# Performance work log

Measured on AMD Instinct MI355X. Metric: run time of the kernel, lower is better.

The kernel has to match this reference:

```python
import jax, jax.numpy as jnp
import numpy as np

N = 50000      # nodes (particles)
E = 1600000    # edges
G = 2000       # graphs (jets)
NEG_SLOPE = 0.2

def setup_inputs() -> dict:
    key = jax.random.key(0)
    ks = jax.random.split(key, 18)
    p = lambda k, s: (jax.random.normal(k, s, jnp.float32) * 0.1)
    return {
        'x': jax.random.normal(ks[0], (N, 3), jnp.float32),
        'edge_index': jax.random.randint(ks[1], (2, E), 0, N, dtype=jnp.int64),
        'batch': jnp.sort(jax.random.randint(ks[2], (N,), 0, G, dtype=jnp.int64)),
        'W1': p(ks[3], (3, 128)),  'a1s': p(ks[4], (4, 32)),  'a1d': p(ks[5], (4, 32)),  'b1': p(ks[6], (128,)),
        'W2': p(ks[7], (128, 128)),'a2s': p(ks[8], (4, 32)),  'a2d': p(ks[9], (4, 32)),  'b2': p(ks[10], (128,)),
        'W3': p(ks[11], (128, 32)),'a3s': p(ks[12], (1, 32)), 'a3d': p(ks[13], (1, 32)), 'b3': p(ks[14], (32,)),
        'Wh': p(ks[15], (32, 2)),  'bh': p(ks[16], (2,)),
    }

def gat_conv(x, src, dst, W, a_src, a_dst, b, concat):
    """PyG GATConv (eval mode): gather-score-softmax-scatter over edges (src->dst)."""
    n = x.shape[0]
    H, C = a_src.shape
    h = (x @ W).reshape(n, H, C)                         # [N,H,C]
    es = jnp.sum(h * a_src, axis=-1)                     # [N,H] source scores
    ed = jnp.sum(h * a_dst, axis=-1)                     # [N,H] dest scores
    e = jax.nn.leaky_relu(es[src] + ed[dst], NEG_SLOPE)  # [E,H]
    # neighbor-wise (per destination node) stable softmax
    m = jax.ops.segment_max(e, dst, num_segments=n)      # [N,H]
    m = jax.lax.stop_gradient(jnp.where(jnp.isfinite(m), m, 0.0))
    w = jnp.exp(e - m[dst])
    z = jax.ops.segment_sum(w, dst, num_segments=n)      # [N,H]
    alpha = w / (z[dst] + 1e-16)                         # [E,H]
    out = jax.ops.segment_sum(h[src] * alpha[:, :, None], dst, num_segments=n)  # [N,H,C]
    out = out.reshape(n, H * C) if concat else out.mean(axis=1)
    return out + b

def reference(x, edge_index, batch, W1, a1s, a1d, b1, W2, a2s, a2d, b2,
              W3, a3s, a3d, b3, Wh, bh):
    n = x.shape[0]
    loops = jnp.arange(n, dtype=edge_index.dtype)        # add_self_loops=True
    src = jnp.concatenate([edge_index[0], loops])
    dst = jnp.concatenate([edge_index[1], loops])
    h = jax.nn.elu(gat_conv(x, src, dst, W1, a1s, a1d, b1, True))
    h = jax.nn.elu(gat_conv(h, src, dst, W2, a2s, a2d, b2, True))
    h = jax.nn.elu(gat_conv(h, src, dst, W3, a3s, a3d, b3, False))
    cnt = jax.ops.segment_sum(jnp.ones((n,), h.dtype), batch, num_segments=G)
    pooled = jax.ops.segment_sum(h, batch, num_segments=G) / jnp.maximum(cnt, 1.0)[:, None]
    return pooled @ Wh + bh                              # [G, n_classes]
```

## Files before the change

kernel.cpp:

```cpp
#include <hip/hip_runtime.h>

#define CAP 80
#define NXCD 8
#define SUBW 128
#define NSUBR 49
#define SQC 96
#define QCAPB 512
#define CHUNK 2048

typedef int vint4 __attribute__((ext_vector_type(4)));
__device__ __forceinline__ vint4 ntload_i4(const int* p){ return __builtin_nontemporal_load((const vint4*)p); }

__device__ __forceinline__ float lrelu02(float x){ return x > 0.f ? x : 0.2f*x; }
__device__ __forceinline__ float eluf(float x){ return x > 0.f ? x : (__expf(x)-1.f); }
__device__ __forceinline__ unsigned short f2bf(float x){
  unsigned u = __float_as_uint(x);
  u += 0x7fffu + ((u >> 16) & 1u);
  return (unsigned short)(u >> 16);
}
__device__ __forceinline__ float bf2f(unsigned short b){
  return __uint_as_float(((unsigned)b) << 16);
}

__global__ void radix_proj1_kernel(const int* __restrict__ src, const int* __restrict__ dst,
                                   int E, int n, int nrb, int RW, int qcap,
                                   int* __restrict__ gcur, int2* __restrict__ qbuf,
                                   const float* __restrict__ x, const float* __restrict__ W,
                                   const float* __restrict__ as_, const float* __restrict__ ad_,
                                   unsigned short* __restrict__ hout, float* __restrict__ es,
                                   float* __restrict__ ed){
  if ((int)blockIdx.x < nrb){
    __shared__ int2 q[NXCD][QCAPB];
    __shared__ int qc[NXCD];
    __shared__ int qbase[NXCD];
    int t = threadIdx.x;
    if (t < NXCD) qc[t] = 0;
    __syncthreads();
    int e0 = blockIdx.x*CHUNK + t*8;
    if (e0 + 8 <= E){
      vint4 d40 = ntload_i4(dst + e0), d41 = ntload_i4(dst + e0 + 4);
      vint4 s40 = ntload_i4(src + e0), s41 = ntload_i4(src + e0 + 4);
      int dd[8] = {d40[0],d40[1],d40[2],d40[3],d41[0],d41[1],d41[2],d41[3]};
      int ss[8] = {s40[0],s40[1],s40[2],s40[3],s41[0],s41[1],s41[2],s41[3]};
      #pragma unroll
      for (int k = 0; k < 8; ++k){
        int qi = min(dd[k] / RW, NXCD-1);
        int pos = atomicAdd(&qc[qi], 1);
        if (pos < QCAPB) q[qi][pos] = make_int2(ss[k], dd[k]);
      }
    } else {
      for (int e = e0; e < E; ++e){
        int d = dst[e];
        int qi = min(d / RW, NXCD-1);
        int pos = atomicAdd(&qc[qi], 1);
        if (pos < QCAPB) q[qi][pos] = make_int2(src[e], d);
      }
    }
    __syncthreads();
    if (t < NXCD) qbase[t] = atomicAdd(&gcur[t], min(qc[t], QCAPB));
    __syncthreads();
    #pragma unroll
    for (int qi = 0; qi < NXCD; ++qi){
      int cq = min(qc[qi], QCAPB);
      int2* gq = qbuf + (size_t)qi*qcap;
      int b0 = qbase[qi];
      for (int i = t; i < cq; i += 256)
        if (b0 + i < qcap) gq[b0 + i] = q[qi][i];
    }
  } else {
    __shared__ float xs[2][3];
    int node0 = ((int)blockIdx.x - nrb) * 2;
    int t = threadIdx.x;
    if (t < 6){
      int nn = node0 + t/3;
      xs[t/3][t%3] = (nn < n) ? x[(size_t)nn*3 + t%3] : 0.f;
    }
    __syncthreads();
    int node = node0 + t / 128;
    int o = t % 128;
    if (node >= n) return;
    const float* xr = xs[t / 128];
    float acc = 0.f;
    #pragma unroll
    for (int k = 0; k < 3; ++k) acc = fmaf(xr[k], W[k*128 + o], acc);
    hout[(size_t)node*128 + o] = f2bf(acc);
    float ts = acc * as_[o];
    float td = acc * ad_[o];
    #pragma unroll
    for (int m = 16; m >= 1; m >>= 1){
      ts += __shfl_xor(ts, m);
      td += __shfl_xor(td, m);
    }
    if ((o & 31) == 0){
      es[node*4 + (o>>5)] = ts;
      ed[node*4 + (o>>5)] = td;
    }
  }
}

__global__ void radix_sub_kernel(const int2* __restrict__ qbuf, const int* __restrict__ gcur,
                                 int qcap, int bpr, int scap,
                                 int* __restrict__ scnt, int2* __restrict__ sbuf){
  __shared__ int2 q[NSUBR][SQC];
  __shared__ int qc[NSUBR];
  __shared__ int qb[NSUBR];
  int r  = blockIdx.x / bpr;
  int bi = blockIdx.x % bpr;
  int t = threadIdx.x;
  if (t < NSUBR) qc[t] = 0;
  __syncthreads();
  int len = min(gcur[r], qcap);
  int i0 = bi*CHUNK + t*8;
  const int2* qg = qbuf + (size_t)r*qcap;
  #pragma unroll
  for (int k = 0; k < 8; ++k){
    int i = i0 + k;
    if (i < len){
      int2 e = qg[i];
      int qi = (e.y >> 7) - r*NSUBR;
      int pos = atomicAdd(&qc[qi], 1);
      if (pos < SQC) q[qi][pos] = e;
    }
  }
  __syncthreads();
  if (t < NSUBR){
    int c = min(qc[t], SQC);
    qb[t] = c ? atomicAdd(&scnt[r*NSUBR + t], c) : 0;
  }
  __syncthreads();
  for (int qi = 0; qi < NSUBR; ++qi){
    int cq = min(qc[qi], SQC);
    if (!cq) continue;
    int2* gq = sbuf + (size_t)(r*NSUBR + qi)*scap;
    int b0 = qb[qi];
    for (int i = t; i < cq; i += 256)
      if (b0 + i < scap) gq[b0 + i] = q[qi][i];
  }
}

__global__ void bucket_csr_kernel(const int2* __restrict__ sbuf, const int* __restrict__ scnt,
                                  int scap, unsigned short* __restrict__ col,
                                  int* __restrict__ deg, int n){
  __shared__ unsigned short colS[SUBW*CAP];
  __shared__ int cur[SUBW];
  int sb = blockIdx.x;
  int t = threadIdx.x;
  {
    uint4 zz = make_uint4(0,0,0,0);
    uint4* cz = (uint4*)colS;
    for (int i = t; i < SUBW*CAP*2/16; i += 256) cz[i] = zz;
  }
  if (t < SUBW) cur[t] = 0;
  __syncthreads();
  int len = min(scnt[sb], scap);
  const int2* sq = sbuf + (size_t)sb*scap;
  for (int i = t; i < len; i += 256){
    int2 e = sq[i];
    int r = e.y & (SUBW-1);
    int slot = atomicAdd(&cur[r], 1);
    if (slot < CAP) colS[r*CAP + slot] = (unsigned short)e.x;
  }
  __syncthreads();
  int base = sb*SUBW;
  int nb = min(SUBW, n - base);
  const uint4* srcp = (const uint4*)colS;
  uint4* dstp = (uint4*)(col + (size_t)base*CAP);
  for (int i = t; i < nb*10; i += 256) dstp[i] = srcp[i];
  if (t < nb) deg[base + t] = min(cur[t], CAP);
}

template<int OUT, int NPT, int H>
__global__ void proj_tiled_kernel(const float* __restrict__ x, const float* __restrict__ W,
                                  const float* __restrict__ as_, const float* __restrict__ ad_,
                                  unsigned short* __restrict__ hout, float* __restrict__ es,
                                  float* __restrict__ ed, int n){
  constexpr int OG = OUT / 4;
  constexpr int NG = 256 / OG;
  constexpr int NODES = NG * NPT;
  __shared__ float xs[128][NODES + 1];
  int node0 = blockIdx.x * NODES;
  int t = threadIdx.x;
  for (int i = t; i < NODES*32; i += 256){
    int nl = i >> 5, kc = i & 31;
    int nn = node0 + nl;
    float4 v = make_float4(0.f,0.f,0.f,0.f);
    if (nn < n) v = *(const float4*)(x + (size_t)nn*128 + kc*4);
    xs[kc*4+0][nl] = v.x;
    xs[kc*4+1][nl] = v.y;
    xs[kc*4+2][nl] = v.z;
    xs[kc*4+3][nl] = v.w;
  }
  __syncthreads();
  int og = t % OG;
  int ng = t / OG;
  float acc[NPT][4];
  #pragma unroll
  for (int p = 0; p < NPT; ++p){ acc[p][0]=0.f; acc[p][1]=0.f; acc[p][2]=0.f; acc[p][3]=0.f; }
  const float* wp = W + og*4;
  #pragma unroll 4
  for (int k = 0; k < 128; ++k){
    float4 w = *(const float4*)(wp + (size_t)k*OUT);
    #pragma unroll
    for (int p = 0; p < NPT; ++p){
      float xv = xs[k][ng*NPT + p];
      acc[p][0] = fmaf(xv, w.x, acc[p][0]);
      acc[p][1] = fmaf(xv, w.y, acc[p][1]);
      acc[p][2] = fmaf(xv, w.z, acc[p][2]);
      acc[p][3] = fmaf(xv, w.w, acc[p][3]);
    }
  }
  int o = og*4;
  float as0 = as_[o], as1 = as_[o+1], as2 = as_[o+2], as3 = as_[o+3];
  float ad0 = ad_[o], ad1 = ad_[o+1], ad2 = ad_[o+2], ad3 = ad_[o+3];
  #pragma unroll
  for (int p = 0; p < NPT; ++p){
    int node = node0 + ng*NPT + p;
    float ts = acc[p][0]*as0 + acc[p][1]*as1 + acc[p][2]*as2 + acc[p][3]*as3;
    float td = acc[p][0]*ad0 + acc[p][1]*ad1 + acc[p][2]*ad2 + acc[p][3]*ad3;
    #pragma unroll
    for (int m = 4; m >= 1; m >>= 1){
      ts += __shfl_xor(ts, m);
      td += __shfl_xor(td, m);
    }
    if (node < n){
      ushort4 hb;
      hb.x = f2bf(acc[p][0]); hb.y = f2bf(acc[p][1]);
      hb.z = f2bf(acc[p][2]); hb.w = f2bf(acc[p][3]);
      *(ushort4*)(hout + (size_t)node*OUT + o) = hb;
      if ((og & 7) == 0){
        int head = og >> 3;
        es[node*H + head] = ts;
        ed[node*H + head] = td;
      }
    }
  }
}

__global__ void agg128_kernel(const unsigned short* __restrict__ h, const float* __restrict__ es,
                              const float* __restrict__ ed, const int* __restrict__ deg,
                              const unsigned short* __restrict__ col, const float* __restrict__ bias,
                              float* __restrict__ out, int n){
  __shared__ float wsS[4][4][CAP];
  int wv = threadIdx.x >> 6;
  int node = blockIdx.x*4 + wv;
  int lane = threadIdx.x & 63;
  if (node >= n) return;
  int beg = node*CAP;
  int degN = min(deg[node], CAP);
  int degR = (degN + 15) & ~15;
  int eh = lane >> 2, hh = lane & 3;
  float edh = ed[node*4 + hh];
  float zp = 0.f;
  for (int base = 0; base < degR; base += 16){
    int e = base + eh;
    float w = 0.f;
    if (e < degN){
      int s = (int)col[beg + e];
      w = __expf(lrelu02(es[s*4 + hh] + edh));
    }
    wsS[wv][hh][e] = w;
    zp += w;
  }
  #pragma unroll
  for (int m = 4; m <= 32; m <<= 1) zp += __shfl_xor(zp, m);
  int head = lane >> 4;
  float z = __shfl(zp, head);
  float ed_h = __shfl(edh, head);
  float a0 = 0.f, a1 = 0.f;
  const unsigned short* colp = col + beg;
  for (int base = 0; base < degR; base += 16){
    uint4 c0 = *(const uint4*)(colp + base);
    uint4 c1 = *(const uint4*)(colp + base + 8);
    unsigned cw[8] = {c0.x,c0.y,c0.z,c0.w,c1.x,c1.y,c1.z,c1.w};
    int s[16];
    #pragma unroll
    for (int k = 0; k < 8; ++k){ s[2*k] = cw[k] & 0xffffu; s[2*k+1] = cw[k] >> 16; }
    float4 w0 = *(const float4*)&wsS[wv][head][base];
    float4 w1 = *(const float4*)&wsS[wv][head][base+4];
    float4 w2 = *(const float4*)&wsS[wv][head][base+8];
    float4 w3 = *(const float4*)&wsS[wv][head][base+12];
    float wk[16] = {w0.x,w0.y,w0.z,w0.w, w1.x,w1.y,w1.z,w1.w,
                    w2.x,w2.y,w2.z,w2.w, w3.x,w3.y,w3.z,w3.w};
    unsigned u[16];
    #pragma unroll
    for (int k = 0; k < 16; ++k) u[k] = *(const unsigned*)(h + (size_t)s[k]*128 + 2*lane);
    #pragma unroll
    for (int k = 0; k < 16; ++k){
      a0 = fmaf(wk[k], __uint_as_float(u[k] << 16), a0);
      a1 = fmaf(wk[k], __uint_as_float(u[k] & 0xffff0000u), a1);
    }
  }
  {
    float w = __expf(lrelu02(es[node*4 + head] + ed_h));
    unsigned u = *(const unsigned*)(h + (size_t)node*128 + 2*lane);
    z += w;
    a0 = fmaf(w, __uint_as_float(u << 16), a0);
    a1 = fmaf(w, __uint_as_float(u & 0xffff0000u), a1);
  }
  float inv = 1.f / (z + 1e-16f);
  int o = 2*lane;
  float2 r;
  r.x = eluf(a0*inv + bias[o]);
  r.y = eluf(a1*inv + bias[o+1]);
  *(float2*)(out + (size_t)node*128 + o) = r;
}

__global__ void agg32_kernel(const unsigned short* __restrict__ h, const float* __restrict__ es,
                             const float* __restrict__ ed, const int* __restrict__ deg,
                             const unsigned short* __restrict__ col, const float* __restrict__ bias,
                             float* __restrict__ out, int n){
  int node = blockIdx.x*4 + (threadIdx.x >> 6);
  int lane = threadIdx.x & 63;
  if (node >= n) return;
  int beg = node*CAP;
  int end = beg + min(deg[node], CAP);
  int half = lane >> 5;
  int c = lane & 31;
  float ed0 = ed[node];
  float a0 = 0.f, z = 0.f;
  int e = beg;
  for (; e + 16 <= end; e += 16){
    uint4 c0 = *(const uint4*)(col + e + 8*half);
    unsigned cw[4] = {c0.x,c0.y,c0.z,c0.w};
    int s[8]; float q[8], hv[8];
    #pragma unroll
    for (int k = 0; k < 4; ++k){ s[2*k] = cw[k] & 0xffffu; s[2*k+1] = cw[k] >> 16; }
    #pragma unroll
    for (int k = 0; k < 8; ++k) q[k] = es[s[k]];
    #pragma unroll
    for (int k = 0; k < 8; ++k) hv[k] = bf2f(h[(size_t)s[k]*32 + c]);
    #pragma unroll
    for (int k = 0; k < 8; ++k){
      float w = __expf(lrelu02(q[k] + ed0));
      z += w;
      a0 = fmaf(w, hv[k], a0);
    }
  }
  for (; e + 2 <= end; e += 2){
    int s = col[e + half];
    float w = __expf(lrelu02(es[s] + ed0));
    float hv = bf2f(h[(size_t)s*32 + c]);
    z += w;
    a0 = fmaf(w, hv, a0);
  }
  if (e < end && half == 0){
    int s = col[e];
    float w = __expf(lrelu02(es[s] + ed0));
    float hv = bf2f(h[(size_t)s*32 + c]);
    z += w;
    a0 = fmaf(w, hv, a0);
  }
  a0 += __shfl_xor(a0, 32);
  z  += __shfl_xor(z, 32);
  {
    float w = __expf(lrelu02(es[node] + ed0));
    float hv = bf2f(h[(size_t)node*32 + c]);
    z += w;
    a0 = fmaf(w, hv, a0);
  }
  if (half == 0){
    float inv = 1.f / (z + 1e-16f);
    out[(size_t)node*32 + c] = eluf(a0*inv + bias[c]);
  }
}

__global__ void pool_kernel(const float* __restrict__ h3, const int* __restrict__ batch,
                            float* __restrict__ pooled, float* __restrict__ cnt, int n){
  int i = blockIdx.x*blockDim.x + threadIdx.x;
  int node = i >> 5, c = i & 31;
  if (node >= n) return;
  int g = batch[node];
  atomicAdd(&pooled[g*32 + c], h3[(size_t)node*32 + c]);
  if (c == 0) atomicAdd(&cnt[g], 1.f);
}

__global__ void head_kernel(const float* __restrict__ pooled, const float* __restrict__ cnt,
                            const float* __restrict__ Wh, const float* __restrict__ bh,
                            float* __restrict__ out, int G){
  int g = blockIdx.x*blockDim.x + threadIdx.x;
  if (g >= G) return;
  float inv = 1.f / fmaxf(cnt[g], 1.f);
  float o0 = bh[0], o1 = bh[1];
  #pragma unroll
  for (int c = 0; c < 32; ++c){
    float p = pooled[g*32 + c] * inv;
    o0 = fmaf(p, Wh[c*2+0], o0);
    o1 = fmaf(p, Wh[c*2+1], o1);
  }
  out[g*2+0] = o0;
  out[g*2+1] = o1;
}

extern "C" void kernel_launch(void* const* d_in, const int* in_sizes, int n_in,
                              void* d_out, int out_size, void* d_ws, size_t ws_size,
                              hipStream_t stream){
  const float* x   = (const float*)d_in[0];
  const int*   ei  = (const int*)d_in[1];
  const int* batch = (const int*)d_in[2];
  const float* W1  = (const float*)d_in[3];
  const float* a1s = (const float*)d_in[4];
  const float* a1d = (const float*)d_in[5];
  const float* b1  = (const float*)d_in[6];
  const float* W2  = (const float*)d_in[7];
  const float* a2s = (const float*)d_in[8];
  const float* a2d = (const float*)d_in[9];
  const float* b2  = (const float*)d_in[10];
  const float* W3  = (const float*)d_in[11];
  const float* a3s = (const float*)d_in[12];
  const float* a3d = (const float*)d_in[13];
  const float* b3  = (const float*)d_in[14];
  const float* Wh  = (const float*)d_in[15];
  const float* bh  = (const float*)d_in[16];
  const int n = in_sizes[0] / 3;
  const int E = in_sizes[1] / 2;
  const int G = out_size / 2;
  float* out = (float*)d_out;

  const int RW   = NSUBR * SUBW;
  const int NSB  = (n + SUBW - 1) / SUBW;
  const int qcap = E/NXCD * 5/4 + 4096;
  const int scap = (int)((long long)E*SUBW/n * 5/4) + 512;

  char* p = (char*)d_ws;
  auto alloc = [&](size_t bytes)->char*{ char* r = p; p += (bytes + 255) & ~(size_t)255; return r; };
  float* buf_x            = (float*)alloc((size_t)n*128*4);
  unsigned short* buf_h   = (unsigned short*)alloc((size_t)n*128*2);
  float* es     = (float*)alloc((size_t)n*4*4);
  float* ed     = (float*)alloc((size_t)n*4*4);
  float* pooled = (float*)alloc((size_t)G*33*4);
  float* cnt    = pooled + (size_t)G*32;
  int* deg      = (int*)alloc((size_t)n*4);
  unsigned short* col = (unsigned short*)alloc((size_t)n*CAP*2);
  int* gcur     = (int*)alloc(NXCD*4);
  int* scnt     = (int*)alloc((size_t)(NXCD*NSUBR)*4);
  int2* qbuf    = (int2*)alloc((size_t)NXCD*qcap*8);
  int2* sbuf    = (int2*)alloc((size_t)NXCD*NSUBR*scap*8);

  const int* srcr = ei;
  const int* dstr = ei + E;

  hipMemsetAsync(gcur, 0, NXCD*4, stream);
  hipMemsetAsync(scnt, 0, (size_t)(NXCD*NSUBR)*4, stream);
  hipMemsetAsync(pooled, 0, (size_t)G*33*4, stream);

  int nrb = (E + CHUNK - 1) / CHUNK;
  int proj_blocks = (n + 1) / 2;
  radix_proj1_kernel<<<nrb + proj_blocks, 256, 0, stream>>>(
      srcr, dstr, E, n, nrb, RW, qcap, gcur, qbuf, x, W1, a1s, a1d, buf_h, es, ed);
  int bpr = (qcap + CHUNK - 1) / CHUNK;
  radix_sub_kernel<<<NXCD*bpr, 256, 0, stream>>>(qbuf, gcur, qcap, bpr, scap, scnt, sbuf);
  bucket_csr_kernel<<<NSB, 256, 0, stream>>>(sbuf, scnt, scap, col, deg, n);

  agg128_kernel<<<(n+3)/4, 256, 0, stream>>>(buf_h, es, ed, deg, col, b1, buf_x, n);
  proj_tiled_kernel<128,4,4><<<(n+31)/32, 256, 0, stream>>>(buf_x, W2, a2s, a2d, buf_h, es, ed, n);
  agg128_kernel<<<(n+3)/4, 256, 0, stream>>>(buf_h, es, ed, deg, col, b2, buf_x, n);
  proj_tiled_kernel<32,2,1><<<(n+63)/64, 256, 0, stream>>>(buf_x, W3, a3s, a3d, buf_h, es, ed, n);
  agg32_kernel<<<(n+3)/4, 256, 0, stream>>>(buf_h, es, ed, deg, col, b3, buf_x, n);

  pool_kernel<<<((n*32)+255)/256, 256, 0, stream>>>(buf_x, batch, pooled, cnt, n);
  head_kernel<<<(G+255)/256, 256, 0, stream>>>(pooled, cnt, Wh, bh, out, G);
}
```

Before: 318.7 us.

## Fuse layer-3 aggregation with mean pooling and precompute edge weights in LDS

```diff
diff --git a/kernel.cpp b/kernel.cpp
--- a/kernel.cpp
+++ b/kernel.cpp
@@ -20,6 +20,11 @@
 }
 __device__ __forceinline__ float bf2f(unsigned short b){
   return __uint_as_float(((unsigned)b) << 16);
+}
+
+__global__ void cnt_kernel(const int* __restrict__ batch, float* __restrict__ cnt, int n){
+  int i = blockIdx.x*blockDim.x + threadIdx.x;
+  if (i < n) atomicAdd(&cnt[batch[i]], 1.f);
 }
 
 __global__ void radix_proj1_kernel(const int* __restrict__ src, const int* __restrict__ dst,
@@ -305,53 +310,54 @@
   *(float2*)(out + (size_t)node*128 + o) = r;
 }
 
-__global__ void agg32_kernel(const unsigned short* __restrict__ h, const float* __restrict__ es,
-                             const float* __restrict__ ed, const int* __restrict__ deg,
-                             const unsigned short* __restrict__ col, const float* __restrict__ bias,
-                             float* __restrict__ out, int n){
-  int node = blockIdx.x*4 + (threadIdx.x >> 6);
+__global__ void agg32_pool_kernel(const unsigned short* __restrict__ h, const float* __restrict__ es,
+                                  const float* __restrict__ ed, const int* __restrict__ deg,
+                                  const unsigned short* __restrict__ col, const float* __restrict__ bias,
+                                  const int* __restrict__ batch, float* __restrict__ pooled, int n){
+  __shared__ float wsS[4][CAP];
+  int wv = threadIdx.x >> 6;
+  int node = blockIdx.x*4 + wv;
   int lane = threadIdx.x & 63;
   if (node >= n) return;
   int beg = node*CAP;
-  int end = beg + min(deg[node], CAP);
+  int degN = min(deg[node], CAP);
+  int degR = (degN + 15) & ~15;
+  float ed0 = ed[node];
+  float zp = 0.f;
+  for (int base = 0; base < CAP; base += 64){
+    int e = base + lane;
+    float w = 0.f;
+    if (e < degN){
+      int s = (int)col[beg + e];
+      w = __expf(lrelu02(es[s] + ed0));
+    }
+    if (e < CAP) wsS[wv][e] = w;
+    zp += w;
+  }
+  #pragma unroll
+  for (int m = 1; m < 64; m <<= 1) zp += __shfl_xor(zp, m);
+  float z = zp;
   int half = lane >> 5;
   int c = lane & 31;
-  float ed0 = ed[node];
-  float a0 = 0.f, z = 0.f;
-  int e = beg;
-  for (; e + 16 <= end; e += 16){
-    uint4 c0 = *(const uint4*)(col + e + 8*half);
-    unsigned cw[4] = {c0.x,c0.y,c0.z,c0.w};
-    int s[8]; float q[8], hv[8];
+  float a0 = 0.f;
+  const unsigned short* colp = col + beg;
+  for (int base = 0; base < degR; base += 16){
+    int b = base + 8*half;
+    uint4 c4 = *(const uint4*)(colp + b);
+    unsigned cw[4] = {c4.x,c4.y,c4.z,c4.w};
+    int s[8];
     #pragma unroll
     for (int k = 0; k < 4; ++k){ s[2*k] = cw[k] & 0xffffu; s[2*k+1] = cw[k] >> 16; }
-    #pragma unroll
-    for (int k = 0; k < 8; ++k) q[k] = es[s[k]];
+    float4 w01 = *(const float4*)&wsS[wv][b];
+    float4 w23 = *(const float4*)&wsS[wv][b+4];
+    float wk[8] = {w01.x,w01.y,w01.z,w01.w, w23.x,w23.y,w23.z,w23.w};
+    float hv[8];
     #pragma unroll
     for (int k = 0; k < 8; ++k) hv[k] = bf2f(h[(size_t)s[k]*32 + c]);
     #pragma unroll
-    for (int k = 0; k < 8; ++k){
-      float w = __expf(lrelu02(q[k] + ed0));
-      z += w;
-      a0 = fmaf(w, hv[k], a0);
-    }
-  }
-  for (; e + 2 <= end; e += 2){
-    int s = col[e + half];
-    float w = __expf(lrelu02(es[s] + ed0));
-    float hv = bf2f(h[(size_t)s*32 + c]);
-    z += w;
-    a0 = fmaf(w, hv, a0);
-  }
-  if (e < end && half == 0){
-    int s = col[e];
-    float w = __expf(lrelu02(es[s] + ed0));
-    float hv = bf2f(h[(size_t)s*32 + c]);
-    z += w;
-    a0 = fmaf(w, hv, a0);
+    for (int k = 0; k < 8; ++k) a0 = fmaf(wk[k], hv[k], a0);
   }
   a0 += __shfl_xor(a0, 32);
-  z  += __shfl_xor(z, 32);
   {
     float w = __expf(lrelu02(es[node] + ed0));
     float hv = bf2f(h[(size_t)node*32 + c]);
@@ -360,18 +366,10 @@
   }
   if (half == 0){
     float inv = 1.f / (z + 1e-16f);
-    out[(size_t)node*32 + c] = eluf(a0*inv + bias[c]);
-  }
-}
-
-__global__ void pool_kernel(const float* __restrict__ h3, const int* __restrict__ batch,
-                            float* __restrict__ pooled, float* __restrict__ cnt, int n){
-  int i = blockIdx.x*blockDim.x + threadIdx.x;
-  int node = i >> 5, c = i & 31;
-  if (node >= n) return;
-  int g = batch[node];
-  atomicAdd(&pooled[g*32 + c], h3[(size_t)node*32 + c]);
-  if (c == 0) atomicAdd(&cnt[g], 1.f);
+    float val = eluf(a0*inv + bias[c]);
+    int g = batch[node];
+    atomicAdd(&pooled[g*32 + c], val);
+  }
 }
 
 __global__ void head_kernel(const float* __restrict__ pooled, const float* __restrict__ cnt,
@@ -443,6 +441,8 @@
   hipMemsetAsync(scnt, 0, (size_t)(NXCD*NSUBR)*4, stream);
   hipMemsetAsync(pooled, 0, (size_t)G*33*4, stream);
 
+  cnt_kernel<<<(n+255)/256, 256, 0, stream>>>(batch, cnt, n);
+
   int nrb = (E + CHUNK - 1) / CHUNK;
   int proj_blocks = (n + 1) / 2;
   radix_proj1_kernel<<<nrb + proj_blocks, 256, 0, stream>>>(
@@ -455,8 +455,7 @@
   proj_tiled_kernel<128,4,4><<<(n+31)/32, 256, 0, stream>>>(buf_x, W2, a2s, a2d, buf_h, es, ed, n);
   agg128_kernel<<<(n+3)/4, 256, 0, stream>>>(buf_h, es, ed, deg, col, b2, buf_x, n);
   proj_tiled_kernel<32,2,1><<<(n+63)/64, 256, 0, stream>>>(buf_x, W3, a3s, a3d, buf_h, es, ed, n);
-  agg32_kernel<<<(n+3)/4, 256, 0, stream>>>(buf_h, es, ed, deg, col, b3, buf_x, n);
-
-  pool_kernel<<<((n*32)+255)/256, 256, 0, stream>>>(buf_x, batch, pooled, cnt, n);
+  agg32_pool_kernel<<<(n+3)/4, 256, 0, stream>>>(buf_h, es, ed, deg, col, b3, batch, pooled, n);
+
   head_kernel<<<(G+255)/256, 256, 0, stream>>>(pooled, cnt, Wh, bh, out, G);
 }
```

Result: faster. 293.2 us (-8.0%).
